# Kernel tuning notes

Measured on AMD Instinct MI355X. Metric: run time of the kernel, lower is better.

Reference implementation:

```python
import jax, jax.numpy as jnp
import numpy as np

BS, T, IN, HS = 512, 2048, 64, 128


def setup_inputs() -> dict:
    key = jax.random.key(0)
    ks = jax.random.split(key, 6)
    stdv = 1.0 / np.sqrt(HS)
    u = lambda k, shape: jax.random.uniform(k, shape, jnp.float32, -stdv, stdv)
    return {
        "x": jax.random.normal(ks[0], (BS, T, IN), jnp.float32),
        "W": u(ks[1], (IN, 4 * HS)),
        "U": u(ks[2], (HS, 4 * HS)),
        "bias": u(ks[3], (4 * HS,)),
        "linear_w": u(ks[4], (1, HS)),
        "linear_b": u(ks[5], (1,)),
    }


def reference(x, W, U, bias, linear_w, linear_b):
    bs = x.shape[0]
    h0 = jnp.zeros((bs, HS), x.dtype)
    c0 = jnp.zeros((bs, HS), x.dtype)

    def step(carry, x_t):
        h, c = carry
        gates = x_t @ W + h @ U + bias  # [bs, 4*HS]
        i_t = jax.nn.sigmoid(gates[:, :HS])
        f_t = jax.nn.sigmoid(gates[:, HS:2 * HS])
        g_t = jnp.tanh(gates[:, 2 * HS:3 * HS])
        o_t = jax.nn.sigmoid(gates[:, 3 * HS:])
        c = f_t * c + i_t * g_t
        h = o_t * jnp.tanh(c)
        return (h, c), None

    xs = jnp.swapaxes(x, 0, 1)  # [T, bs, IN]
    (h_t, c_t), _ = jax.lax.scan(step, (h0, c0), xs)
    y_t = h_t @ linear_w.T + linear_b  # [bs, 1]
    return (y_t, h_t, c_t)
```

## Files before the change

kernel.cpp:

```cpp
#include <hip/hip_runtime.h>


#define T_STEPS 2048
#define IN_DIM 64
#define HS 128
#define NG 512
#define ROWS 2
#define NBLK 256
#define NTHR 512
#define CH 32
#define NCH (T_STEPS / CH)
#define HROW 144

typedef float f32x4 __attribute__((ext_vector_type(4)));
typedef short s16x8 __attribute__((ext_vector_type(8)));
typedef int   i32x4 __attribute__((ext_vector_type(4)));

__device__ __forceinline__ unsigned f2bf(float f) {
  unsigned u = __float_as_uint(f);
  return (u + 0x7fffu + ((u >> 16) & 1u)) >> 16;
}
__device__ __forceinline__ float bf2f(unsigned short s) {
  return __int_as_float(((int)s) << 16);
}
__device__ __forceinline__ float rcpf(float x) { return __builtin_amdgcn_rcpf(x); }
__device__ __forceinline__ float sigm(float x) { return rcpf(1.0f + __expf(-x)); }
__device__ __forceinline__ float tanhfast(float x) {
  return 1.0f - 2.0f * rcpf(__expf(2.0f * x) + 1.0f);
}
__device__ __forceinline__ int xswz(int f) { return f ^ (((f >> 7) & 7) << 3); }

__global__ __launch_bounds__(NTHR, 1)
void lstm_fused(const float* __restrict__ X, const float* __restrict__ W,
                const float* __restrict__ U, const float* __restrict__ B,
                const float* __restrict__ LW, const float* __restrict__ LB,
                float* __restrict__ OUT) {
  __shared__ __align__(16) short Zc[CH * 128 * 8];
  __shared__ __align__(16) float Xl[4096];
  __shared__ __align__(16) unsigned char Hq[2][ROWS * HROW];
  __shared__ float Ys[256];
  __shared__ float Ps[8];

  const int tid  = threadIdx.x;
  const int lane = tid & 63;
  const int w    = tid >> 6;
  const int blk  = blockIdx.x;
  const int lrow = lane & 15;
  const int lg   = lane >> 4;
  const int col8 = (w * 16 + lrow) * 8;

  i32x4 bUq[4][2];
  float scl[4];
  s16x8 bfrW[4][2];
  float biasg[4];
#pragma unroll
  for (int n = 0; n < 4; ++n) {
    const int p = n * HS + w * 16 + lrow;
    float m = 1e-8f;
    for (int k = 0; k < HS; ++k) m = fmaxf(m, fabsf(U[k * NG + p]));
    const float su = m / 127.f;
    const float rsu = 127.f / m;
    scl[n] = su * (1.f / 127.f);
#pragma unroll
    for (int kt = 0; kt < 2; ++kt) {
      int vq[4] = {0, 0, 0, 0};
      for (int j = 0; j < 16; ++j) {
        const int k = kt * 64 + (lg << 4) + j;
        int q = (int)rintf(U[k * NG + p] * rsu);
        q = q < -127 ? -127 : (q > 127 ? 127 : q);
        vq[j >> 2] |= (q & 0xff) << ((j & 3) * 8);
      }
      bUq[n][kt] = (i32x4){vq[0], vq[1], vq[2], vq[3]};
    }
#pragma unroll
    for (int kt = 0; kt < 2; ++kt)
#pragma unroll
      for (int j = 0; j < 8; ++j)
        bfrW[n][kt][j] = (short)f2bf(W[(kt * 32 + (lg << 3) + j) * NG + p]);
    biasg[n] = B[p];
  }

  f32x4 sx0, sx1, sx2, sx3;
  auto stage_load = [&](int cc) {
    if (w < 4) {
#pragma unroll
      for (int q = 0; q < 4; ++q) {
        const int f   = w * 1024 + q * 256 + lane * 4;
        const int tlc = f >> 7;
        const int row = (f >> 6) & 1;
        const int k   = f & 63;
        const f32x4 v = *(const f32x4*)(
            X + ((long)(blk * ROWS + row) * T_STEPS + (long)cc * CH + tlc) * IN_DIM + k);
        if (q == 0) sx0 = v; else if (q == 1) sx1 = v;
        else if (q == 2) sx2 = v; else sx3 = v;
      }
    }
  };
  auto stage_write = [&]() {
    if (w < 4) {
#pragma unroll
      for (int q = 0; q < 4; ++q) {
        const int f = w * 1024 + q * 256 + lane * 4;
        const f32x4 v = (q == 0) ? sx0 : (q == 1) ? sx1 : (q == 2) ? sx2 : sx3;
        *(f32x4*)&Xl[xswz(f)] = v;
      }
    }
  };

  stage_load(0);
  stage_write();
  for (int i = tid; i < 2 * ROWS * HROW; i += NTHR) ((unsigned char*)Hq)[i] = 0;

  i32x4 afr[2];
  const i32x4 izer = {0, 0, 0, 0};
  afr[0] = izer; afr[1] = izer;

  float creg = 0.f, hreg = 0.f;
  __syncthreads();

#pragma unroll 1
  for (int c = 0; c < NCH; ++c) {
#pragma unroll
    for (int mt = 0; mt < 4; ++mt) {
      const int fb = mt * 1024 + (lrow >> 1) * 128 + (lrow & 1) * 64;
      const int f0 = xswz(fb + 8 * lg);
      const int f1 = xswz(fb + 32 + 8 * lg);
      const f32x4 x0 = *(const f32x4*)&Xl[f0];
      const f32x4 x1 = *(const f32x4*)&Xl[f0 + 4];
      const f32x4 x2 = *(const f32x4*)&Xl[f1];
      const f32x4 x3 = *(const f32x4*)&Xl[f1 + 4];
      s16x8 a0, a1;
#pragma unroll
      for (int j = 0; j < 4; ++j) {
        a0[j] = (short)f2bf(x0[j]); a0[4 + j] = (short)f2bf(x1[j]);
        a1[j] = (short)f2bf(x2[j]); a1[4 + j] = (short)f2bf(x3[j]);
      }
      f32x4 ac[4];
#pragma unroll
      for (int n = 0; n < 4; ++n) {
        ac[n][0] = biasg[n]; ac[n][1] = biasg[n];
        ac[n][2] = biasg[n]; ac[n][3] = biasg[n];
      }
#pragma unroll
      for (int n = 0; n < 4; ++n)
        ac[n] = __builtin_amdgcn_mfma_f32_16x16x32_bf16(a0, bfrW[n][0], ac[n], 0, 0, 0);
#pragma unroll
      for (int n = 0; n < 4; ++n)
        ac[n] = __builtin_amdgcn_mfma_f32_16x16x32_bf16(a1, bfrW[n][1], ac[n], 0, 0, 0);
      s16x8 z0, z1;
#pragma unroll
      for (int n = 0; n < 4; ++n) {
        z0[n] = (short)f2bf(ac[n][0]); z0[4 + n] = (short)f2bf(ac[n][1]);
        z1[n] = (short)f2bf(ac[n][2]); z1[4 + n] = (short)f2bf(ac[n][3]);
      }
      const int tl0 = mt * 8 + 2 * lg;
      *(s16x8*)&Zc[tl0 * 1024 + col8]       = z0;
      *(s16x8*)&Zc[(tl0 + 1) * 1024 + col8] = z1;
    }
    __syncthreads();
    stage_load((c + 1 < NCH) ? c + 1 : c);

#pragma unroll 1
    for (int tl = 0; tl < CH; ++tl) {
      const int t = c * CH + tl;
      const s16x8 zc = *(const s16x8*)&Zc[tl * 1024 + col8];

      i32x4 acc[4];
#pragma unroll
      for (int n = 0; n < 4; ++n) acc[n] = izer;

      __builtin_amdgcn_s_setprio(1);
#pragma unroll
      for (int kt = 0; kt < 2; ++kt) {
        acc[0] = __builtin_amdgcn_mfma_i32_16x16x64_i8(afr[kt], bUq[0][kt], acc[0], 0, 0, 0);
        acc[2] = __builtin_amdgcn_mfma_i32_16x16x64_i8(afr[kt], bUq[2][kt], acc[2], 0, 0, 0);
        acc[1] = __builtin_amdgcn_mfma_i32_16x16x64_i8(afr[kt], bUq[1][kt], acc[1], 0, 0, 0);
        acc[3] = __builtin_amdgcn_mfma_i32_16x16x64_i8(afr[kt], bUq[3][kt], acc[3], 0, 0, 0);
      }
      __builtin_amdgcn_s_setprio(0);

      if (tl == 4) stage_write();

      const int hi16 = lane & 16;
      const int q0 = __builtin_amdgcn_ds_swizzle(acc[0][1], 0x401F);
      const int q2 = __builtin_amdgcn_ds_swizzle(acc[2][1], 0x401F);
      const float v0 = (float)(hi16 ? q0 : acc[0][0]) * scl[0]
                     + bf2f((unsigned short)(hi16 ? zc[4] : zc[0]));
      const float v2 = (float)(hi16 ? q2 : acc[2][0]) * scl[2]
                     + bf2f((unsigned short)(hi16 ? zc[6] : zc[2]));
      const float iv = sigm(v0), gv = tanhfast(v2);
      const float pg = iv * gv;
      const int q1 = __builtin_amdgcn_ds_swizzle(acc[1][1], 0x401F);
      const int q3 = __builtin_amdgcn_ds_swizzle(acc[3][1], 0x401F);
      const float v1 = (float)(hi16 ? q1 : acc[1][0]) * scl[1]
                     + bf2f((unsigned short)(hi16 ? zc[5] : zc[1]));
      const float v3 = (float)(hi16 ? q3 : acc[3][0]) * scl[3]
                     + bf2f((unsigned short)(hi16 ? zc[7] : zc[3]));
      const float fv = sigm(v1), ov = sigm(v3);
      creg = fv * creg + pg;
      hreg = ov * tanhfast(creg);

      if (lane < 32) {
        const int colc = w * 16 + lrow;
        const int r    = lg & 1;
        if (t < T_STEPS - 1) {
          const int hq = (int)rintf(hreg * 127.f);
          Hq[(t + 1) & 1][r * HROW + colc] = (unsigned char)hq;
        } else {
          const int row = blk * ROWS + r;
          OUT[512 + row * HS + colc]   = hreg;
          OUT[66048 + row * HS + colc] = creg;
          Ys[r * HS + colc] = LW[colc] * hreg;
        }
      }
      __syncthreads();

      if (t < T_STEPS - 1 && lrow < ROWS) {
        const unsigned char* hb = &Hq[(t + 1) & 1][lrow * HROW];
        afr[0] = *(const i32x4*)&hb[lg << 4];
        afr[1] = *(const i32x4*)&hb[64 + (lg << 4)];
      }
    }
  }

  if (tid < 8) {
    const int r = tid >> 2, seg = tid & 3;
    float s = 0.f;
#pragma unroll 8
    for (int j = 0; j < 32; ++j) s += Ys[r * 128 + seg * 32 + j];
    Ps[tid] = s;
  }
  __syncthreads();
  if (tid < ROWS) {
    OUT[blk * ROWS + tid] = LB[0] + Ps[tid * 4] + Ps[tid * 4 + 1]
                                  + Ps[tid * 4 + 2] + Ps[tid * 4 + 3];
  }
}

extern "C" void kernel_launch(void* const* d_in, const int* in_sizes, int n_in,
                              void* d_out, int out_size, void* d_ws, size_t ws_size,
                              hipStream_t stream) {
  const float* X  = (const float*)d_in[0];
  const float* W  = (const float*)d_in[1];
  const float* U  = (const float*)d_in[2];
  const float* B  = (const float*)d_in[3];
  const float* LW = (const float*)d_in[4];
  const float* LB = (const float*)d_in[5];
  lstm_fused<<<dim3(NBLK), dim3(NTHR), 0, stream>>>(X, W, U, B, LW, LB, (float*)d_out);
}
```

Before: 1.056 ms.

## Split LSTM gate activations across half-waves and relayout hidden-state rows

Batch rows are remapped into MFMA A-rows 0 and 4 so both rows land in the j=0 accumulator slot. That lets the low half-wave compute the input and cell gates while the high half-wave computes the forget and output gates, with data exchanged through ds_bpermute. Tanh is rewritten as a scaled sigmoid so both halves run the same instruction sequence, and the packed pre-activation load is narrowed to the two values each lane needs. The aim is to cut per-lane transcendental work and cross-lane swizzles on the serial per-timestep critical path. The cost is an extra bpermute round trip before the cell update.

```diff
diff --git a/kernel.cpp b/kernel.cpp
--- a/kernel.cpp
+++ b/kernel.cpp
@@ -20,11 +20,7 @@
   unsigned u = __float_as_uint(f);
   return (u + 0x7fffu + ((u >> 16) & 1u)) >> 16;
 }
-__device__ __forceinline__ float bf2f(unsigned short s) {
-  return __int_as_float(((int)s) << 16);
-}
 __device__ __forceinline__ float rcpf(float x) { return __builtin_amdgcn_rcpf(x); }
-__device__ __forceinline__ float sigm(float x) { return rcpf(1.0f + __expf(-x)); }
 __device__ __forceinline__ float tanhfast(float x) {
   return 1.0f - 2.0f * rcpf(__expf(2.0f * x) + 1.0f);
 }
@@ -37,7 +33,7 @@
                 float* __restrict__ OUT) {
   __shared__ __align__(16) short Zc[CH * 128 * 8];
   __shared__ __align__(16) float Xl[4096];
-  __shared__ __align__(16) unsigned char Hq[2][ROWS * HROW];
+  __shared__ __align__(16) unsigned char Hq[2][2][HROW];
   __shared__ float Ys[256];
   __shared__ float Ps[8];
 
@@ -48,6 +44,8 @@
   const int lrow = lane & 15;
   const int lg   = lane >> 4;
   const int col8 = (w * 16 + lrow) * 8;
+  const bool low = (lane < 32);
+  const int bidx = (lane & 31) << 2;
 
   i32x4 bUq[4][2];
   float scl[4];
@@ -58,9 +56,8 @@
     const int p = n * HS + w * 16 + lrow;
     float m = 1e-8f;
     for (int k = 0; k < HS; ++k) m = fmaxf(m, fabsf(U[k * NG + p]));
-    const float su = m / 127.f;
     const float rsu = 127.f / m;
-    scl[n] = su * (1.f / 127.f);
+    scl[n] = m / (127.f * 127.f);
 #pragma unroll
     for (int kt = 0; kt < 2; ++kt) {
       int vq[4] = {0, 0, 0, 0};
@@ -79,6 +76,11 @@
         bfrW[n][kt][j] = (short)f2bf(W[(kt * 32 + (lg << 3) + j) * NG + p]);
     biasg[n] = B[p];
   }
+  const float sA = low ? scl[0] : scl[1];
+  const float sB = low ? scl[2] : scl[3];
+  const float cA = low ? -2.f : -1.f;
+  const float cB = low ?  2.f :  1.f;
+  const float cC = low ? -1.f :  0.f;
 
   f32x4 sx0, sx1, sx2, sx3;
   auto stage_load = [&](int cc) {
@@ -109,7 +111,7 @@
 
   stage_load(0);
   stage_write();
-  for (int i = tid; i < 2 * ROWS * HROW; i += NTHR) ((unsigned char*)Hq)[i] = 0;
+  for (int i = tid; i < 2 * 2 * HROW; i += NTHR) ((unsigned char*)Hq)[i] = 0;
 
   i32x4 afr[2];
   const i32x4 izer = {0, 0, 0, 0};
@@ -163,7 +165,7 @@
 #pragma unroll 1
     for (int tl = 0; tl < CH; ++tl) {
       const int t = c * CH + tl;
-      const s16x8 zc = *(const s16x8*)&Zc[tl * 1024 + col8];
+      const uint2 zu = *(const uint2*)&Zc[tl * 1024 + col8 + (lg & 1) * 4];
 
       i32x4 acc[4];
 #pragma unroll
@@ -172,40 +174,39 @@
       __builtin_amdgcn_s_setprio(1);
 #pragma unroll
       for (int kt = 0; kt < 2; ++kt) {
+        acc[1] = __builtin_amdgcn_mfma_i32_16x16x64_i8(afr[kt], bUq[1][kt], acc[1], 0, 0, 0);
+        acc[3] = __builtin_amdgcn_mfma_i32_16x16x64_i8(afr[kt], bUq[3][kt], acc[3], 0, 0, 0);
         acc[0] = __builtin_amdgcn_mfma_i32_16x16x64_i8(afr[kt], bUq[0][kt], acc[0], 0, 0, 0);
         acc[2] = __builtin_amdgcn_mfma_i32_16x16x64_i8(afr[kt], bUq[2][kt], acc[2], 0, 0, 0);
-        acc[1] = __builtin_amdgcn_mfma_i32_16x16x64_i8(afr[kt], bUq[1][kt], acc[1], 0, 0, 0);
-        acc[3] = __builtin_amdgcn_mfma_i32_16x16x64_i8(afr[kt], bUq[3][kt], acc[3], 0, 0, 0);
       }
       __builtin_amdgcn_s_setprio(0);
 
       if (tl == 4) stage_write();
 
-      const int hi16 = lane & 16;
-      const int q0 = __builtin_amdgcn_ds_swizzle(acc[0][1], 0x401F);
-      const int q2 = __builtin_amdgcn_ds_swizzle(acc[2][1], 0x401F);
-      const float v0 = (float)(hi16 ? q0 : acc[0][0]) * scl[0]
-                     + bf2f((unsigned short)(hi16 ? zc[4] : zc[0]));
-      const float v2 = (float)(hi16 ? q2 : acc[2][0]) * scl[2]
-                     + bf2f((unsigned short)(hi16 ? zc[6] : zc[2]));
-      const float iv = sigm(v0), gv = tanhfast(v2);
-      const float pg = iv * gv;
-      const int q1 = __builtin_amdgcn_ds_swizzle(acc[1][1], 0x401F);
-      const int q3 = __builtin_amdgcn_ds_swizzle(acc[3][1], 0x401F);
-      const float v1 = (float)(hi16 ? q1 : acc[1][0]) * scl[1]
-                     + bf2f((unsigned short)(hi16 ? zc[5] : zc[1]));
-      const float v3 = (float)(hi16 ? q3 : acc[3][0]) * scl[3]
-                     + bf2f((unsigned short)(hi16 ? zc[7] : zc[3]));
-      const float fv = sigm(v1), ov = sigm(v3);
-      creg = fv * creg + pg;
-      hreg = ov * tanhfast(creg);
-
-      if (lane < 32) {
-        const int colc = w * 16 + lrow;
-        const int r    = lg & 1;
+      const int r1 = __builtin_amdgcn_ds_bpermute(bidx, acc[1][0]);
+      const int r3 = __builtin_amdgcn_ds_bpermute(bidx, acc[3][0]);
+      const int a02 = low ? acc[0][0] : r1;
+      const int a13 = low ? acc[2][0] : r3;
+      const float zA = __int_as_float(low ? (zu.x << 16) : (zu.x & 0xffff0000u));
+      const float zB = __int_as_float(low ? (zu.y << 16) : (zu.y & 0xffff0000u));
+      const float vA = (float)a02 * sA + zA;
+      const float vB = (float)a13 * sB + zB;
+      const float g1 = rcpf(1.f + __expf(-vA));
+      const float g2 = cB * rcpf(1.f + __expf(cA * vB)) + cC;
+      const float pg = g1 * g2;
+      const float pgp = __int_as_float(
+          __builtin_amdgcn_ds_bpermute(bidx, __float_as_int(pg)));
+      creg = g1 * creg + pgp;
+      const float tc = tanhfast(creg);
+      hreg = g2 * tc;
+
+      if (lane >= 32) {
+        const int b    = lane - 32;
+        const int colc = w * 16 + (b & 15);
+        const int r    = b >> 4;
         if (t < T_STEPS - 1) {
           const int hq = (int)rintf(hreg * 127.f);
-          Hq[(t + 1) & 1][r * HROW + colc] = (unsigned char)hq;
+          Hq[(t + 1) & 1][r][colc] = (unsigned char)hq;
         } else {
           const int row = blk * ROWS + r;
           OUT[512 + row * HS + colc]   = hreg;
@@ -215,8 +216,8 @@
       }
       __syncthreads();
 
-      if (t < T_STEPS - 1 && lrow < ROWS) {
-        const unsigned char* hb = &Hq[(t + 1) & 1][lrow * HROW];
+      if (t < T_STEPS - 1 && (lrow & 3) == 0 && lrow < 8) {
+        const unsigned char* hb = Hq[(t + 1) & 1][lrow >> 2];
         afr[0] = *(const i32x4*)&hb[lg << 4];
         afr[1] = *(const i32x4*)&hb[64 + (lg << 4)];
       }
```

New measurement: 1.034 ms. 1.02x faster.
